# Kernel tuning notes

Hardware: AMD Instinct MI355X
Metric: run time of the kernel (lower is better)

Reference implementation:

```python
import jax, jax.numpy as jnp
import numpy as np

RCUT = 6.0
BOX = 8.0  # box edge so a good fraction of random pairs fall inside rcut


def setup_inputs() -> dict:
    key = jax.random.key(0)
    k1, k2, k3, k4, k5 = jax.random.split(key, 5)
    nframes, nloc, nnei, nall, ntypes, nspline = 8, 8192, 128, 16384, 4, 2000
    extended_coord = jax.random.uniform(k1, (nframes, nall, 3), dtype=jnp.float32) * BOX
    extended_atype = jax.random.randint(k2, (nframes, nall), 0, ntypes, dtype=jnp.int64)
    nlist = jax.random.randint(k3, (nframes, nloc, nnei), 0, nall, dtype=jnp.int64)
    pad = jax.random.uniform(k4, (nframes, nloc, nnei)) < 0.2
    nlist = jnp.where(pad, jnp.asarray(-1, nlist.dtype), nlist)
    tab_data = jax.random.normal(k5, (ntypes, ntypes, nspline, 4), dtype=jnp.float32) * 0.1
    # tab_info = [rmin, hh, nspline, ntypes]; table spans [0, 10] > rcut
    tab_info = jnp.array([0.0, 0.005, float(nspline), float(ntypes)], dtype=jnp.float32)
    return {
        "extended_coord": extended_coord,
        "tab_data": tab_data,
        "tab_info": tab_info,
        "extended_atype": extended_atype,
        "nlist": nlist,
    }


def reference(extended_coord, tab_data, tab_info, extended_atype, nlist):
    nframes, nloc, nnei = nlist.shape
    nspline = tab_data.shape[2]  # static
    rmin, hh = tab_info[0], tab_info[1]

    mask = nlist >= 0
    mnlist = jnp.where(mask, nlist, 0)

    i_type = extended_atype[:, :nloc]                                  # (nf, nloc)
    flat = mnlist.reshape(nframes, nloc * nnei)
    j_type = jnp.take_along_axis(extended_atype, flat, axis=1).reshape(nframes, nloc, nnei)

    # pairwise distances via neighbor gather
    coord_l = extended_coord[:, :nloc, None, :]                        # (nf, nloc, 1, 3)
    coord_r = jnp.take_along_axis(extended_coord, flat[:, :, None], axis=1)
    coord_r = coord_r.reshape(nframes, nloc, nnei, 3)
    rr = jnp.linalg.norm(coord_r - coord_l, axis=-1)                   # (nf, nloc, nnei)

    # table coordinate; padded slots pushed past table end
    uu = (rr - rmin) / hh
    uu = jnp.where(mask, uu, jnp.asarray(nspline + 1, uu.dtype))
    idx = uu.astype(jnp.int32)
    uu = uu - idx

    # gather cubic-spline coefficients indexed by (i_type, j_type, bin)
    clip = jnp.clip(idx, 0, nspline - 1)
    ii = jnp.broadcast_to(i_type[:, :, None], j_type.shape)
    coef = tab_data[ii, j_type, clip]                                   # (nf, nloc, nnei, 4)
    coef = jnp.where((idx > nspline)[..., None], jnp.zeros((), coef.dtype), coef)

    a3, a2, a1, a0 = coef[..., 0], coef[..., 1], coef[..., 2], coef[..., 3]
    ener = ((a3 * uu + a2) * uu + a1) * uu + a0

    beyond = (rr >= RCUT) | (rr >= rmin + nspline * hh)
    ener = jnp.where(beyond, jnp.zeros((), ener.dtype), ener)

    atomic_energy = 0.5 * jnp.sum(jnp.where(mask, ener, jnp.zeros((), ener.dtype)), axis=-1, keepdims=True)
    return atomic_energy  # (nf, nloc, 1)
```

## Files before the change

### kernel.cpp

```cpp
#include <hip/hip_runtime.h>

constexpr int NFRAMES = 8;
constexpr int NLOC    = 8192;
constexpr int NNEI    = 128;
constexpr int NALL    = 16384;
constexpr int NTYPES  = 4;
constexpr int NSPLINE = 2000;
constexpr int KLIVE   = 1200;
constexpr int KBLK    = 8;

#define FP_BAR(x) asm volatile("" : "+v"(x))

__global__ __launch_bounds__(256) void pack_kernel(
    const float* __restrict__ coord, const int* __restrict__ atype,
    float4* __restrict__ pack, int* __restrict__ cnts)
{
    int t = blockIdx.x * 256 + threadIdx.x;
    if (blockIdx.x == 0 && threadIdx.x < NFRAMES * NTYPES) cnts[threadIdx.x] = 0;
    float4 v;
    v.x = coord[3 * (size_t)t + 0];
    v.y = coord[3 * (size_t)t + 1];
    v.z = coord[3 * (size_t)t + 2];
    v.w = __int_as_float(atype[t]);
    pack[t] = v;
}

__global__ __launch_bounds__(256) void bucket_kernel(
    const int* __restrict__ atype, int* __restrict__ perm,
    int* __restrict__ cnts)
{
    __shared__ int hist[NTYPES];
    __shared__ int base[NTYPES];
    const int t = blockIdx.x * 256 + threadIdx.x;
    const int f = t >> 13;
    const int i = t & (NLOC - 1);
    const int ty = atype[(size_t)f * NALL + i];

    if (threadIdx.x < NTYPES) hist[threadIdx.x] = 0;
    __syncthreads();
    const int my_off = atomicAdd(&hist[ty], 1);
    __syncthreads();
    if (threadIdx.x < NTYPES)
        base[threadIdx.x] = atomicAdd(&cnts[f * NTYPES + threadIdx.x],
                                      hist[threadIdx.x]);
    __syncthreads();
    perm[(size_t)(f * NTYPES + ty) * NLOC + base[ty] + my_off] = i;
}

__device__ __forceinline__ double nb_energy_lds(
    float4 c, bool valid, float xl, float yl, float zl,
    float rmin, float recip, const float4* __restrict__ ltab)
{
    float dx = c.x - xl;  FP_BAR(dx);
    float dy = c.y - yl;  FP_BAR(dy);
    float dz = c.z - zl;  FP_BAR(dz);
    float my = dy * dy;                    FP_BAR(my);
    float t1 = __builtin_fmaf(dx, dx, my); FP_BAR(t1);
    float ss = __builtin_fmaf(dz, dz, t1); FP_BAR(ss);
    float rr = sqrtf(ss);                  FP_BAR(rr);
    float num = rr - rmin;               FP_BAR(num);
    float uu  = num * recip;             FP_BAR(uu);
    double e = 0.0;
    if (valid && rr < 6.0f) {
        int    idx = (int)uu;
        double t   = (double)uu - (double)idx;
        int    tj  = __float_as_int(c.w);
        float4 cf  = ltab[tj * KLIVE + idx];
        e = (((double)cf.x * t + (double)cf.y) * t + (double)cf.z) * t
            + (double)cf.w;
    }
    return e;
}

__global__ __launch_bounds__(1024, 8) void pairtab_lds_kernel(
    const float4* __restrict__ pack,
    const float*  __restrict__ tab,
    const float*  __restrict__ tab_info,
    const int*    __restrict__ nlist,
    const int*    __restrict__ perm,
    const int*    __restrict__ cnts,
    float*        __restrict__ out)
{
    __shared__ float4 ltab[NTYPES * KLIVE];

    const int bucket = blockIdx.x >> 3;
    const int chunk  = blockIdx.x & (KBLK - 1);
    const int f  = bucket >> 2;
    const int ti = bucket & 3;

    const float4* tsrc = (const float4*)tab + (size_t)ti * (NTYPES * NSPLINE);
    for (int idx = threadIdx.x; idx < NTYPES * KLIVE; idx += 1024) {
        int tj = idx / KLIVE;
        int k  = idx - tj * KLIVE;
        ltab[idx] = tsrc[tj * NSPLINE + k];
    }
    __syncthreads();

    const float rmin = tab_info[0];
    const float hh   = tab_info[1];
    float recip = (float)(1.0 / (double)hh);  FP_BAR(recip);

    const int cnt  = cnts[bucket];
    const int lane = threadIdx.x & 63;
    const int wave = (int)(threadIdx.x >> 6);
    const int half = lane >> 5;
    const int lih  = lane & 31;
    const size_t fb = (size_t)f * NALL;
    const int* __restrict__ permb = perm + (size_t)bucket * NLOC;
    const int* __restrict__ nlf   = nlist + (size_t)f * NLOC * NNEI;
    const float4 zero4 = make_float4(0.f, 0.f, 0.f, 0.f);

    for (int s0 = chunk * 32; s0 < cnt; s0 += KBLK * 32) {
        const int s = s0 + wave * 2 + half;
        const bool active = s < cnt;
        const int loc = active ? permb[s] : 0;

        const float4 pl = pack[fb + loc];
        const float xl = pl.x, yl = pl.y, zl = pl.z;

        const int4 jj = ((const int4*)(nlf + (size_t)loc * NNEI))[lih];

        float4 c0 = zero4, c1 = zero4, c2 = zero4, c3 = zero4;
        if (jj.x >= 0) c0 = pack[fb + jj.x];
        if (jj.y >= 0) c1 = pack[fb + jj.y];
        if (jj.z >= 0) c2 = pack[fb + jj.z];
        if (jj.w >= 0) c3 = pack[fb + jj.w];

        double esum = nb_energy_lds(c0, jj.x >= 0, xl, yl, zl, rmin, recip, ltab)
                    + nb_energy_lds(c1, jj.y >= 0, xl, yl, zl, rmin, recip, ltab)
                    + nb_energy_lds(c2, jj.z >= 0, xl, yl, zl, rmin, recip, ltab)
                    + nb_energy_lds(c3, jj.w >= 0, xl, yl, zl, rmin, recip, ltab);

#pragma unroll
        for (int off = 16; off >= 1; off >>= 1)
            esum += __shfl_xor(esum, off, 64);

        if (active && lih == 0) out[(size_t)f * NLOC + loc] = (float)(0.5 * esum);
    }
}

__device__ __forceinline__ double nb_energy_g(
    float4 c, bool valid, float xl, float yl, float zl,
    float rmin, float recip, const float* __restrict__ tabi)
{
    float dx = c.x - xl;  FP_BAR(dx);
    float dy = c.y - yl;  FP_BAR(dy);
    float dz = c.z - zl;  FP_BAR(dz);
    float my = dy * dy;                    FP_BAR(my);
    float t1 = __builtin_fmaf(dx, dx, my); FP_BAR(t1);
    float ss = __builtin_fmaf(dz, dz, t1); FP_BAR(ss);
    float rr = sqrtf(ss);                  FP_BAR(rr);
    float num = rr - rmin;               FP_BAR(num);
    float uu  = num * recip;             FP_BAR(uu);
    int   idx = (int)uu;
    double t  = (double)uu - (double)idx;
    int clip  = idx < 0 ? 0 : (idx > NSPLINE - 1 ? NSPLINE - 1 : idx);
    int tj    = __float_as_int(c.w);
    const float4 coef =
        *(const float4*)(tabi + (((size_t)tj * NSPLINE + clip) << 2));
    double e = (((double)coef.x * t + (double)coef.y) * t + (double)coef.z) * t
               + (double)coef.w;
    bool zero = (!valid) | (idx > NSPLINE) | (rr >= 6.0f);
    return zero ? 0.0 : e;
}

__global__ __launch_bounds__(256) void pairtab_kernel(
    const float4* __restrict__ pack, const float* __restrict__ tab,
    const float* __restrict__ tab_info, const int* __restrict__ nlist,
    float* __restrict__ out)
{
    const int lane = threadIdx.x & 63;
    const int wid  = (blockIdx.x * 256 + threadIdx.x) >> 6;
    const int half = lane >> 5;
    const int gloc = 2 * wid + half;
    const int f = gloc >> 13;
    const int i = gloc & (NLOC - 1);
    const float rmin = tab_info[0];
    const float hh   = tab_info[1];
    float recip = (float)(1.0 / (double)hh);  FP_BAR(recip);
    const float4 pl = pack[(size_t)f * NALL + i];
    const float xl = pl.x, yl = pl.y, zl = pl.z;
    const int   ti = __float_as_int(pl.w);
    const float* tabi = tab + (size_t)ti * (NTYPES * NSPLINE * 4);
    const int4 jj = ((const int4*)(nlist + (size_t)wid * 256))[lane];
    const int mj0 = jj.x < 0 ? 0 : jj.x, mj1 = jj.y < 0 ? 0 : jj.y;
    const int mj2 = jj.z < 0 ? 0 : jj.z, mj3 = jj.w < 0 ? 0 : jj.w;
    const size_t fb = (size_t)f * NALL;
    const float4 c0 = pack[fb + mj0], c1 = pack[fb + mj1];
    const float4 c2 = pack[fb + mj2], c3 = pack[fb + mj3];
    double esum = nb_energy_g(c0, jj.x >= 0, xl, yl, zl, rmin, recip, tabi)
                + nb_energy_g(c1, jj.y >= 0, xl, yl, zl, rmin, recip, tabi)
                + nb_energy_g(c2, jj.z >= 0, xl, yl, zl, rmin, recip, tabi)
                + nb_energy_g(c3, jj.w >= 0, xl, yl, zl, rmin, recip, tabi);
#pragma unroll
    for (int off = 16; off >= 1; off >>= 1)
        esum += __shfl_xor(esum, off, 64);
    if ((lane & 31) == 0) out[gloc] = (float)(0.5 * esum);
}

extern "C" void kernel_launch(void* const* d_in, const int* in_sizes, int n_in,
                              void* d_out, int out_size, void* d_ws, size_t ws_size,
                              hipStream_t stream)
{
    const float* coord   = (const float*)d_in[0];
    const float* tab     = (const float*)d_in[1];
    const float* tabinfo = (const float*)d_in[2];
    const int*   atype   = (const int*)d_in[3];
    const int*   nlist   = (const int*)d_in[4];
    float* out  = (float*)d_out;

    float4* pack = (float4*)d_ws;
    int*    perm = (int*)((char*)d_ws + 2 * 1024 * 1024);
    int*    cnts = (int*)((char*)d_ws + 3 * 1024 * 1024);
    const size_t need = 3 * 1024 * 1024 + 128;

    pack_kernel<<<(NFRAMES * NALL) / 256, 256, 0, stream>>>(coord, atype, pack,
                                                            cnts);
    if (ws_size >= need) {
        bucket_kernel<<<(NFRAMES * NLOC) / 256, 256, 0, stream>>>(atype, perm, cnts);
        pairtab_lds_kernel<<<NFRAMES * NTYPES * KBLK, 1024, 0, stream>>>(
            pack, tab, tabinfo, nlist, perm, cnts, out);
    } else {
        pairtab_kernel<<<(NFRAMES * NLOC) / 8, 256, 0, stream>>>(
            pack, tab, tabinfo, nlist, out);
    }
}
```

Before: 116.0 us.

## Chunk neighbor coordinates into LDS using compacted 16-bit per-chunk neighbor lists

Adds a compaction pass that splits each atom's neighbor list by 4096-atom coordinate chunk and stores 16-bit local indices with per-chunk offsets. The main kernel then stages each coordinate chunk in shared memory next to the spline table and gathers neighbors from LDS instead of global memory, keeping per-row partial sums in registers across chunks. The aim is to replace scattered global gathers with LDS reads. In exchange it adds a full extra pass over the neighbor list, four block-wide sync rounds, heavy LDS use that limits occupancy to one large block per CU, and it only runs when the workspace is at least about 20 MB.

```diff
diff --git a/kernel.cpp b/kernel.cpp
--- a/kernel.cpp
+++ b/kernel.cpp
@@ -8,6 +8,12 @@
 constexpr int NSPLINE = 2000;
 constexpr int KLIVE   = 1200;
 constexpr int KBLK    = 8;
+
+constexpr int CHUNK   = 4096;
+constexpr int NCHUNK  = NALL / CHUNK;
+constexpr int SLICES2 = 8;
+constexpr int ITN     = 16;
+constexpr int OVN     = 16;
 
 #define FP_BAR(x) asm volatile("" : "+v"(x))
 
@@ -45,6 +51,35 @@
                                       hist[threadIdx.x]);
     __syncthreads();
     perm[(size_t)(f * NTYPES + ty) * NLOC + base[ty] + my_off] = i;
+}
+
+__global__ __launch_bounds__(256) void compact_kernel(
+    const int* __restrict__ nlist, ushort* __restrict__ cl,
+    int4* __restrict__ offs)
+{
+    const int w    = (blockIdx.x * 256 + threadIdx.x) >> 6;
+    const int lane = threadIdx.x & 63;
+    const int* __restrict__ row = nlist + (size_t)w * NNEI;
+    ushort* __restrict__ crow = cl + (size_t)w * NNEI;
+    const int j0 = row[lane];
+    const int j1 = row[64 + lane];
+    const unsigned long long lt = (1ull << lane) - 1ull;
+    int base = 0;
+    int e[NCHUNK];
+#pragma unroll
+    for (int c = 0; c < NCHUNK; ++c) {
+        const bool m0 = (j0 >= 0) && ((j0 >> 12) == c);
+        const bool m1 = (j1 >= 0) && ((j1 >> 12) == c);
+        const unsigned long long b0 = __ballot(m0);
+        const unsigned long long b1 = __ballot(m1);
+        const int n0 = __popcll(b0);
+        if (m0) crow[base + __popcll(b0 & lt)] = (ushort)(j0 & (CHUNK - 1));
+        if (m1) crow[base + n0 + __popcll(b1 & lt)] =
+            (ushort)(j1 & (CHUNK - 1));
+        base += n0 + __popcll(b1);
+        e[c] = base;
+    }
+    if (lane == 0) offs[w] = make_int4(e[0], e[1], e[2], e[3]);
 }
 
 __device__ __forceinline__ double nb_energy_lds(
@@ -70,6 +105,134 @@
             + (double)cf.w;
     }
     return e;
+}
+
+__device__ __forceinline__ double row_chunk_energy(
+    int c, const int4 pe, const ushort* __restrict__ crow,
+    const float4 pl, int lih, float rmin, float recip,
+    const float4* __restrict__ cpack, const float4* __restrict__ ltab)
+{
+    const int beg = (c == 0) ? 0 : ((c == 1) ? pe.x : ((c == 2) ? pe.y : pe.z));
+    const int end = (c == 0) ? pe.x
+                             : ((c == 1) ? pe.y : ((c == 2) ? pe.z : pe.w));
+    double es = 0.0;
+    for (int b = beg; b < end; b += 32) {
+        const bool lv = (b + lih) < end;
+        float4 cc = make_float4(0.f, 0.f, 0.f, 0.f);
+        if (lv) cc = cpack[crow[b + lih]];
+        es += nb_energy_lds(cc, lv, pl.x, pl.y, pl.z, rmin, recip, ltab);
+    }
+    return es;
+}
+
+__global__ __launch_bounds__(1024) void pairtab_chunk_kernel(
+    const float4* __restrict__ pack,
+    const float*  __restrict__ tab,
+    const float*  __restrict__ tab_info,
+    const ushort* __restrict__ cl,
+    const int4*   __restrict__ offs,
+    const int*    __restrict__ perm,
+    const int*    __restrict__ cnts,
+    float*        __restrict__ out)
+{
+    __shared__ float4 ltab[NTYPES * KLIVE];
+    __shared__ float4 cpack[CHUNK];
+    __shared__ double accov[OVN * 32];
+
+    const int bucket = blockIdx.x >> 3;
+    const int slice  = blockIdx.x & (SLICES2 - 1);
+    const int f  = bucket >> 2;
+    const int ti = bucket & 3;
+
+    const float4* tsrc = (const float4*)tab + (size_t)ti * (NTYPES * NSPLINE);
+    for (int idx = threadIdx.x; idx < NTYPES * KLIVE; idx += 1024) {
+        int tj = idx / KLIVE;
+        int k  = idx - tj * KLIVE;
+        ltab[idx] = tsrc[tj * NSPLINE + k];
+    }
+    if (threadIdx.x < OVN * 32) accov[threadIdx.x] = 0.0;
+
+    const float rmin = tab_info[0];
+    const float hh   = tab_info[1];
+    float recip = (float)(1.0 / (double)hh);  FP_BAR(recip);
+
+    const int cnt  = cnts[bucket];
+    const int lane = threadIdx.x & 63;
+    const int wave = (int)(threadIdx.x >> 6);
+    const int half = lane >> 5;
+    const int lih  = lane & 31;
+    const int slot = (wave << 1) | half;
+    const size_t fb = (size_t)f * NALL;
+    const int*    __restrict__ permb = perm + (size_t)bucket * NLOC;
+    const int4*   __restrict__ offf  = offs + (size_t)f * NLOC;
+    const ushort* __restrict__ clf   = cl   + (size_t)f * NLOC * NNEI;
+
+    double eacc[ITN];
+#pragma unroll
+    for (int i = 0; i < ITN; ++i) eacc[i] = 0.0;
+
+#pragma unroll 1
+    for (int c = 0; c < NCHUNK; ++c) {
+        __syncthreads();
+        {
+            const float4* psrc = pack + fb + c * CHUNK;
+            for (int k = threadIdx.x; k < CHUNK; k += 1024) cpack[k] = psrc[k];
+        }
+        __syncthreads();
+
+#pragma unroll
+        for (int it = 0; it < ITN; ++it) {
+            const int s = slice * 32 + it * (SLICES2 * 32) + slot;
+            if (s < cnt) {
+                const int loc = permb[s];
+                eacc[it] += row_chunk_energy(c, offf[loc],
+                                             clf + (size_t)loc * NNEI,
+                                             pack[fb + loc], lih, rmin, recip,
+                                             cpack, ltab);
+            }
+        }
+
+        int ov = 0;
+        for (int s0 = slice * 32 + ITN * (SLICES2 * 32); s0 < cnt;
+             s0 += SLICES2 * 32, ++ov) {
+            const int s = s0 + slot;
+            double es = 0.0;
+            if (s < cnt) {
+                const int loc = permb[s];
+                es = row_chunk_energy(c, offf[loc], clf + (size_t)loc * NNEI,
+                                      pack[fb + loc], lih, rmin, recip,
+                                      cpack, ltab);
+            }
+#pragma unroll
+            for (int off = 16; off >= 1; off >>= 1)
+                es += __shfl_xor(es, off, 64);
+            if (s < cnt && lih == 0) accov[ov * 32 + slot] += es;
+        }
+    }
+    __syncthreads();
+
+#pragma unroll
+    for (int it = 0; it < ITN; ++it) {
+        const int s = slice * 32 + it * (SLICES2 * 32) + slot;
+        if (s < cnt) {
+            double es = eacc[it];
+#pragma unroll
+            for (int off = 16; off >= 1; off >>= 1)
+                es += __shfl_xor(es, off, 64);
+            if (lih == 0)
+                out[(size_t)f * NLOC + permb[s]] = (float)(0.5 * es);
+        }
+    }
+    {
+        int ov = 0;
+        for (int s0 = slice * 32 + ITN * (SLICES2 * 32); s0 < cnt;
+             s0 += SLICES2 * 32, ++ov) {
+            const int s = s0 + slot;
+            if (s < cnt && lih == 0)
+                out[(size_t)f * NLOC + permb[s]] =
+                    (float)(0.5 * accov[ov * 32 + slot]);
+        }
+    }
 }
 
 __global__ __launch_bounds__(1024, 8) void pairtab_lds_kernel(
@@ -212,12 +375,23 @@
     float4* pack = (float4*)d_ws;
     int*    perm = (int*)((char*)d_ws + 2 * 1024 * 1024);
     int*    cnts = (int*)((char*)d_ws + 3 * 1024 * 1024);
-    const size_t need = 3 * 1024 * 1024 + 128;
+    int4*   offs = (int4*)((char*)d_ws + 3 * 1024 * 1024 + 4096);
+    ushort* cl16 = (ushort*)((char*)d_ws + 4 * 1024 * 1024 + 4096);
+    const size_t need3 = 20 * 1024 * 1024 + 8192;
+    const size_t need1 = 3 * 1024 * 1024 + 128;
 
     pack_kernel<<<(NFRAMES * NALL) / 256, 256, 0, stream>>>(coord, atype, pack,
                                                             cnts);
-    if (ws_size >= need) {
-        bucket_kernel<<<(NFRAMES * NLOC) / 256, 256, 0, stream>>>(atype, perm, cnts);
+    if (ws_size >= need3) {
+        bucket_kernel<<<(NFRAMES * NLOC) / 256, 256, 0, stream>>>(atype, perm,
+                                                                  cnts);
+        compact_kernel<<<(NFRAMES * NLOC) / 4, 256, 0, stream>>>(nlist, cl16,
+                                                                 offs);
+        pairtab_chunk_kernel<<<NFRAMES * NTYPES * SLICES2, 1024, 0, stream>>>(
+            pack, tab, tabinfo, cl16, offs, perm, cnts, out);
+    } else if (ws_size >= need1) {
+        bucket_kernel<<<(NFRAMES * NLOC) / 256, 256, 0, stream>>>(atype, perm,
+                                                                  cnts);
         pairtab_lds_kernel<<<NFRAMES * NTYPES * KBLK, 1024, 0, stream>>>(
             pack, tab, tabinfo, nlist, perm, cnts, out);
     } else {
```

New measurement: 141.0 us. +21.5%, slower.

## Stage neighbor coordinates in LDS by chunk with compacted 16-bit neighbor lists

Applied to the files above, without the earlier changes.

Adds a compaction kernel that splits each neighbor row into 4096-atom chunks of extended atoms and stores the entries as 16-bit local indices, with per-chunk offsets. The main kernel now assigns one block per (frame, type, chunk, slice), copies that chunk's packed coordinates into shared memory and reads neighbors from LDS instead of making scattered global gathers. Partial energies are combined with float atomicAdd into an output zeroed in the pack kernel, and the next atom's metadata is prefetched. The cost is an extra kernel launch, a larger workspace requirement, atomic traffic, and a summation order that can vary between runs.

```diff
diff --git a/kernel.cpp b/kernel.cpp
--- a/kernel.cpp
+++ b/kernel.cpp
@@ -9,14 +9,20 @@
 constexpr int KLIVE   = 1200;
 constexpr int KBLK    = 8;
 
+constexpr int CHUNK   = 4096;
+constexpr int NCHUNK  = NALL / CHUNK;
+constexpr int SLICES  = 2;
+
 #define FP_BAR(x) asm volatile("" : "+v"(x))
 
 __global__ __launch_bounds__(256) void pack_kernel(
     const float* __restrict__ coord, const int* __restrict__ atype,
-    float4* __restrict__ pack, int* __restrict__ cnts)
+    float4* __restrict__ pack, int* __restrict__ cnts,
+    float* __restrict__ outz)
 {
     int t = blockIdx.x * 256 + threadIdx.x;
     if (blockIdx.x == 0 && threadIdx.x < NFRAMES * NTYPES) cnts[threadIdx.x] = 0;
+    if (t < NFRAMES * NLOC) outz[t] = 0.f;
     float4 v;
     v.x = coord[3 * (size_t)t + 0];
     v.y = coord[3 * (size_t)t + 1];
@@ -45,6 +51,47 @@
                                       hist[threadIdx.x]);
     __syncthreads();
     perm[(size_t)(f * NTYPES + ty) * NLOC + base[ty] + my_off] = i;
+}
+
+__global__ __launch_bounds__(256) void compact_kernel(
+    const int* __restrict__ nlist, ushort* __restrict__ cl,
+    int4* __restrict__ offs)
+{
+    __shared__ alignas(16) ushort srow[8][128];
+    const int hr  = threadIdx.x >> 5;
+    const int lih = threadIdx.x & 31;
+    const int w   = blockIdx.x * 8 + hr;
+    const int* __restrict__ row = nlist + (size_t)w * NNEI;
+    const int4 j4 = ((const int4*)row)[lih];
+    const uint lt = (1u << lih) - 1u;
+    const int hsh = (hr & 1) * 32;
+    int base = 0;
+    int e[NCHUNK];
+#pragma unroll
+    for (int c = 0; c < NCHUNK; ++c) {
+        const bool m0 = (j4.x >= 0) && ((j4.x >> 12) == c);
+        const bool m1 = (j4.y >= 0) && ((j4.y >> 12) == c);
+        const bool m2 = (j4.z >= 0) && ((j4.z >> 12) == c);
+        const bool m3 = (j4.w >= 0) && ((j4.w >> 12) == c);
+        const uint b0 = (uint)(__ballot(m0) >> hsh);
+        const uint b1 = (uint)(__ballot(m1) >> hsh);
+        const uint b2 = (uint)(__ballot(m2) >> hsh);
+        const uint b3 = (uint)(__ballot(m3) >> hsh);
+        const int n0 = __popc(b0), n1 = __popc(b1), n2 = __popc(b2);
+        if (m0) srow[hr][base + __popc(b0 & lt)] = (ushort)(j4.x & (CHUNK - 1));
+        if (m1) srow[hr][base + n0 + __popc(b1 & lt)] =
+            (ushort)(j4.y & (CHUNK - 1));
+        if (m2) srow[hr][base + n0 + n1 + __popc(b2 & lt)] =
+            (ushort)(j4.z & (CHUNK - 1));
+        if (m3) srow[hr][base + n0 + n1 + n2 + __popc(b3 & lt)] =
+            (ushort)(j4.w & (CHUNK - 1));
+        base += n0 + n1 + n2 + __popc(b3);
+        e[c] = base;
+    }
+    __syncthreads();
+    if (lih < 16)
+        ((int4*)(cl + (size_t)w * NNEI))[lih] = ((const int4*)srow[hr])[lih];
+    if (lih == 0) offs[w] = make_int4(e[0], e[1], e[2], e[3]);
 }
 
 __device__ __forceinline__ double nb_energy_lds(
@@ -70,6 +117,109 @@
             + (double)cf.w;
     }
     return e;
+}
+
+__global__ __launch_bounds__(1024) void pairtab_stream_kernel(
+    const float4* __restrict__ pack,
+    const float*  __restrict__ tab,
+    const float*  __restrict__ tab_info,
+    const ushort* __restrict__ cl,
+    const int4*   __restrict__ offs,
+    const int*    __restrict__ perm,
+    const int*    __restrict__ cnts,
+    float*        __restrict__ out)
+{
+    __shared__ float4 ltab[NTYPES * KLIVE];
+    __shared__ float4 cpack[CHUNK];
+
+    const int blk    = blockIdx.x;
+    const int slice  = blk & (SLICES - 1);
+    const int c      = (blk >> 1) & (NCHUNK - 1);
+    const int bucket = blk >> 3;
+    const int f  = bucket >> 2;
+    const int ti = bucket & 3;
+
+    const float4* tsrc = (const float4*)tab + (size_t)ti * (NTYPES * NSPLINE);
+    for (int idx = threadIdx.x; idx < NTYPES * KLIVE; idx += 1024) {
+        int tj = idx / KLIVE;
+        int k  = idx - tj * KLIVE;
+        ltab[idx] = tsrc[tj * NSPLINE + k];
+    }
+    {
+        const float4* psrc = pack + (size_t)f * NALL + c * CHUNK;
+        for (int k = threadIdx.x; k < CHUNK; k += 1024) cpack[k] = psrc[k];
+    }
+    __syncthreads();
+
+    const float rmin = tab_info[0];
+    const float hh   = tab_info[1];
+    float recip = (float)(1.0 / (double)hh);  FP_BAR(recip);
+
+    const int cnt  = cnts[bucket];
+    const int lane = threadIdx.x & 63;
+    const int wave = (int)(threadIdx.x >> 6);
+    const int half = lane >> 5;
+    const int lih  = lane & 31;
+    const int slot = (wave << 1) | half;
+    const size_t fb = (size_t)f * NALL;
+    const int*    __restrict__ permb = perm + (size_t)bucket * NLOC;
+    const int4*   __restrict__ offf  = offs + (size_t)f * NLOC;
+    const ushort* __restrict__ clf   = cl   + (size_t)f * NLOC * NNEI;
+    const float4 zero4 = make_float4(0.f, 0.f, 0.f, 0.f);
+
+    int s = 2 * slot + slice;
+    int loc = 0; int4 pe = make_int4(0, 0, 0, 0); float4 pl = zero4;
+    if (s < cnt) {
+        loc = permb[s];
+        pe  = offf[loc];
+        pl  = pack[fb + loc];
+    }
+    while (s < cnt) {
+        const int sn = s + 64;
+        int locn = 0; int4 pen = make_int4(0, 0, 0, 0); float4 pln = zero4;
+        if (sn < cnt) {
+            locn = permb[sn];
+            pen  = offf[locn];
+            pln  = pack[fb + locn];
+        }
+
+        const int beg = (c == 0) ? 0
+                      : ((c == 1) ? pe.x : ((c == 2) ? pe.y : pe.z));
+        const int end = (c == 0) ? pe.x
+                      : ((c == 1) ? pe.y : ((c == 2) ? pe.z : pe.w));
+        const ushort* __restrict__ crow = clf + (size_t)loc * NNEI;
+
+        const int A  = beg & ~7;
+        const int nw = (end - A + 7) >> 3;
+        int4 v = make_int4(0, 0, 0, 0);
+        if (lih < nw) v = ((const int4*)(crow + A))[lih];
+
+        double es = 0.0;
+        const int ng = (end - beg + 31) >> 5;
+        for (int g = 0; g < ng; ++g) {
+            const int off  = (beg & 7) + (g << 5) + lih;
+            const bool lv  = (beg + (g << 5) + lih) < end;
+            const int srcl = (half << 5) + (off >> 3);
+            const int a0 = __shfl(v.x, srcl, 64);
+            const int a1 = __shfl(v.y, srcl, 64);
+            const int a2 = __shfl(v.z, srcl, 64);
+            const int a3 = __shfl(v.w, srcl, 64);
+            const int d  = (off >> 1) & 3;
+            const int wd = (d == 0) ? a0 : ((d == 1) ? a1 : ((d == 2) ? a2 : a3));
+            const int us = (off & 1) ? ((wd >> 16) & 0xffff) : (wd & 0xffff);
+            float4 cc = zero4;
+            if (lv) cc = cpack[us];
+            es += nb_energy_lds(cc, lv, pl.x, pl.y, pl.z, rmin, recip, ltab);
+        }
+
+#pragma unroll
+        for (int o = 16; o >= 1; o >>= 1)
+            es += __shfl_xor(es, o, 64);
+        if (lih == 0)
+            atomicAdd(&out[(size_t)f * NLOC + loc], (float)(0.5 * es));
+
+        s = sn; loc = locn; pe = pen; pl = pln;
+    }
 }
 
 __global__ __launch_bounds__(1024, 8) void pairtab_lds_kernel(
@@ -212,12 +362,24 @@
     float4* pack = (float4*)d_ws;
     int*    perm = (int*)((char*)d_ws + 2 * 1024 * 1024);
     int*    cnts = (int*)((char*)d_ws + 3 * 1024 * 1024);
-    const size_t need = 3 * 1024 * 1024 + 128;
+    int4*   offs = (int4*)((char*)d_ws + 3 * 1024 * 1024 + 4096);
+    ushort* cl16 = (ushort*)((char*)d_ws + 4 * 1024 * 1024 + 4096);
+    const size_t need3 = 20 * 1024 * 1024 + 8192;
+    const size_t need1 = 3 * 1024 * 1024 + 128;
 
     pack_kernel<<<(NFRAMES * NALL) / 256, 256, 0, stream>>>(coord, atype, pack,
-                                                            cnts);
-    if (ws_size >= need) {
-        bucket_kernel<<<(NFRAMES * NLOC) / 256, 256, 0, stream>>>(atype, perm, cnts);
+                                                            cnts, out);
+    if (ws_size >= need3) {
+        bucket_kernel<<<(NFRAMES * NLOC) / 256, 256, 0, stream>>>(atype, perm,
+                                                                  cnts);
+        compact_kernel<<<(NFRAMES * NLOC) / 8, 256, 0, stream>>>(nlist, cl16,
+                                                                 offs);
+        pairtab_stream_kernel<<<NFRAMES * NTYPES * NCHUNK * SLICES, 1024, 0,
+                                stream>>>(
+            pack, tab, tabinfo, cl16, offs, perm, cnts, out);
+    } else if (ws_size >= need1) {
+        bucket_kernel<<<(NFRAMES * NLOC) / 256, 256, 0, stream>>>(atype, perm,
+                                                                  cnts);
         pairtab_lds_kernel<<<NFRAMES * NTYPES * KBLK, 1024, 0, stream>>>(
             pack, tab, tabinfo, nlist, perm, cnts, out);
     } else {
```

New measurement: 159.7 us. +37.6%, slower.
